# Performance work log

Hardware: AMD Instinct MI355X
Metric: run time of the kernel (lower is better)

The kernel has to match this reference:

```python
import jax, jax.numpy as jnp
import numpy as np

B, N_V, N_H, K = 16384, 4096, 1024, 3
LR, MOMENTUM, WEIGHT_DECAY = 1e-3, 0.5, 1e-4


def setup_inputs() -> dict:
    key = jax.random.key(0)
    k1, k2, k3, k4 = jax.random.split(key, 4)
    inputs = jax.random.uniform(k1, (B, N_V), dtype=jnp.float32)
    weights = jax.random.normal(k2, (N_V, N_H), dtype=jnp.float32) * 0.1
    visible_bias = jnp.ones((N_V,), jnp.float32) * 0.5
    hidden_bias = jnp.zeros((N_H,), jnp.float32)
    weights_momentum = jnp.zeros((N_V, N_H), jnp.float32)
    visible_bias_momentum = jnp.zeros((N_V,), jnp.float32)
    hidden_bias_momentum = jnp.zeros((N_H,), jnp.float32)
    # one uniform vector of length n_hidden per sampling step (matches torch code)
    rand_h0 = jax.random.uniform(k3, (N_H,), dtype=jnp.float32)
    rand_hk = jax.random.uniform(k4, (K, N_H), dtype=jnp.float32)
    return {
        "inputs": inputs,
        "weights": weights,
        "visible_bias": visible_bias,
        "hidden_bias": hidden_bias,
        "weights_momentum": weights_momentum,
        "visible_bias_momentum": visible_bias_momentum,
        "hidden_bias_momentum": hidden_bias_momentum,
        "rand_h0": rand_h0,
        "rand_hk": rand_hk,
    }


def reference(inputs, weights, visible_bias, hidden_bias,
              weights_momentum, visible_bias_momentum, hidden_bias_momentum,
              rand_h0, rand_hk):
    dtype = inputs.dtype

    def sample_hidden(v):  # [B,V] -> [B,H]
        return jax.nn.sigmoid(v @ weights + hidden_bias)

    def sample_visible(h):  # [B,H] -> [B,V]
        return jax.nn.sigmoid(h @ weights.T + visible_bias)

    # positive phase
    pos_hidden_probs = sample_hidden(inputs)                      # [B,H]
    pos_hidden_acts = (pos_hidden_probs >= rand_h0).astype(dtype)  # [B,H]
    pos_associations = inputs.T @ pos_hidden_acts                 # [V,H]

    # negative phase (CD-k). NOTE: in the original torch code `hid_acts` is
    # never updated inside the k-1 loop, so every iteration recomputes the
    # identical visible_probs/hidden_probs from pos_hidden_acts; the extra
    # bernoulli draws (rand_hk) only feed hidden_acts, which is discarded.
    # The final values are therefore exactly one reconstruction step:
    neg_visible_probs = sample_visible(pos_hidden_acts)           # [B,V]
    neg_hidden_probs = sample_hidden(neg_visible_probs)           # [B,H]
    neg_associations = neg_visible_probs.T @ neg_hidden_probs     # [V,H]

    # momentum optimizer step
    batch_size = inputs.shape[0]
    w_mom = weights_momentum * MOMENTUM + (pos_associations - neg_associations)
    vb_mom = visible_bias_momentum * MOMENTUM + jnp.sum(inputs - neg_visible_probs, axis=0)
    hb_mom = hidden_bias_momentum * MOMENTUM + jnp.sum(pos_hidden_probs - neg_hidden_probs, axis=0)

    new_weights = weights + w_mom * (LR / batch_size)
    new_weights = new_weights - new_weights * WEIGHT_DECAY
    new_visible_bias = visible_bias + vb_mom * (LR / batch_size)
    new_hidden_bias = hidden_bias + hb_mom * (LR / batch_size)

    # reconstruction error (original has a bug using builtin `input`; intended `inputs`)
    error = jnp.sum((inputs - neg_visible_probs) ** 2)
    return (error, new_weights, new_visible_bias, new_hidden_bias)
```

## Files before the change

### kernel.cpp

```cpp
#include <hip/hip_runtime.h>
#include <hip/hip_bf16.h>

#define DEV __device__ __forceinline__

typedef __attribute__((ext_vector_type(8))) short bhalf8;
typedef __attribute__((ext_vector_type(4))) float floatx4;
typedef unsigned short ushort_t;

constexpr int NB = 16384;
constexpr int NV = 4096;
constexpr int NH = 1024;
constexpr float MOM = 0.5f;
constexpr float WD  = 1e-4f;
constexpr float LRB = 1e-3f / 16384.0f;

constexpr int BUF_SHORTS = 12288;
constexpr int LDS_SHORTS = 3 * BUF_SHORTS;
constexpr size_t LDS_BYTES = LDS_SHORTS * 2 + 1024 + 64;

DEV unsigned short f2bf(float f) {
  unsigned u = __builtin_bit_cast(unsigned, f);
  u += 0x7FFFu + ((u >> 16) & 1u);
  return (unsigned short)(u >> 16);
}
DEV float bf2f(unsigned short u) {
  unsigned x = ((unsigned)u) << 16;
  return __builtin_bit_cast(float, x);
}
DEV float sigm(float x) { return 1.0f / (1.0f + __expf(-x)); }

DEV void gl16(const ushort_t* g, ushort_t* l) {
  __builtin_amdgcn_global_load_lds(
      (const __attribute__((address_space(1))) void*)g,
      (__attribute__((address_space(3))) void*)l,
      16, 0, 0);
}

struct TransLds { unsigned U[64 * 33]; };

DEV void trans_store(TransLds& T, const bhalf8& ra, const bhalf8& rb, int a, int e) {
  const unsigned* ua = (const unsigned*)&ra;
  const unsigned* ub = (const unsigned*)&rb;
#pragma unroll
  for (int c2 = 0; c2 < 4; ++c2) {
    unsigned lo = __builtin_amdgcn_perm(ub[c2], ua[c2], 0x05040100u);
    unsigned hi = __builtin_amdgcn_perm(ub[c2], ua[c2], 0x07060302u);
    T.U[(e * 8 + 2 * c2) * 33 + a] = lo;
    T.U[(e * 8 + 2 * c2 + 1) * 33 + a] = hi;
  }
}

DEV void trans_flush(const TransLds& T, ushort_t* __restrict__ oT,
                     int c0, int r0, int R, int tid) {
  const int g = tid >> 2, f = tid & 3;
  unsigned w[8];
#pragma unroll
  for (int i = 0; i < 8; ++i) w[i] = T.U[g * 33 + f * 8 + i];
  ushort_t* dst = oT + (size_t)(c0 + g) * R + r0 + f * 16;
  *(bhalf8*)dst = *(const bhalf8*)&w[0];
  *(bhalf8*)(dst + 8) = *(const bhalf8*)&w[4];
}

__global__ void prep_cvt_t(const float* __restrict__ in,
                           ushort_t* __restrict__ obf,
                           ushort_t* __restrict__ oT, int R, int C,
                           float* __restrict__ pin) {
  __shared__ TransLds T;
  __shared__ float wp[4][64];
  const int c0 = blockIdx.x * 64, r0 = blockIdx.y * 64;
  const int tid = threadIdx.x;
  const int a = tid >> 3, e = tid & 7;
  const int rA = r0 + 2 * a, cB = c0 + e * 8;

  const float* pA = in + (size_t)rA * C + cB;
  const float* pB = pA + C;
  floatx4 a0 = *(const floatx4*)pA, a1 = *(const floatx4*)(pA + 4);
  floatx4 b0 = *(const floatx4*)pB, b1 = *(const floatx4*)(pB + 4);

  bhalf8 ra, rb;
#pragma unroll
  for (int j = 0; j < 4; ++j) {
    ra[j] = (short)f2bf(a0[j]); ra[4 + j] = (short)f2bf(a1[j]);
    rb[j] = (short)f2bf(b0[j]); rb[4 + j] = (short)f2bf(b1[j]);
  }
  *(bhalf8*)(obf + (size_t)rA * C + cB) = ra;
  *(bhalf8*)(obf + (size_t)(rA + 1) * C + cB) = rb;

  if (pin) {
    float ps[8];
#pragma unroll
    for (int j = 0; j < 4; ++j) { ps[j] = a0[j] + b0[j]; ps[4 + j] = a1[j] + b1[j]; }
#pragma unroll
    for (int j = 0; j < 8; ++j) {
      ps[j] += __shfl_xor(ps[j], 8);
      ps[j] += __shfl_xor(ps[j], 16);
      ps[j] += __shfl_xor(ps[j], 32);
    }
    const int wid = tid >> 6, lane = tid & 63;
    if (lane < 8) {
#pragma unroll
      for (int j = 0; j < 8; ++j) wp[wid][lane * 8 + j] = ps[j];
    }
  }

  trans_store(T, ra, rb, a, e);
  __syncthreads();
  trans_flush(T, oT, c0, r0, R, tid);
  if (pin && tid < 64) {
    pin[(size_t)blockIdx.y * C + c0 + tid] =
        wp[0][tid] + wp[1][tid] + wp[2][tid] + wp[3][tid];
  }
}

__global__ void transb(const ushort_t* __restrict__ in,
                       ushort_t* __restrict__ out, int R, int C) {
  __shared__ TransLds T;
  const int c0 = blockIdx.x * 64, r0 = blockIdx.y * 64;
  const int tid = threadIdx.x;
  const int a = tid >> 3, e = tid & 7;
  const int rA = r0 + 2 * a, cB = c0 + e * 8;
  bhalf8 ra = *(const bhalf8*)(in + (size_t)rA * C + cB);
  bhalf8 rb = *(const bhalf8*)(in + (size_t)(rA + 1) * C + cB);
  trans_store(T, ra, rb, a, e);
  __syncthreads();
  trans_flush(T, out, c0, r0, R, tid);
}

DEV void core(const ushort_t* __restrict__ Ap,
              const ushort_t* __restrict__ Bp,
              size_t ldA, size_t ldB, int nt,
              ushort_t* Lp, int wid, int lane, int wm, int wn,
              floatx4 (&acc)[8][4]) {
  const int lr = lane & 15, kg = lane >> 4;
  const int sslot = ((lane & 3) ^ (((lane & 32) ? 2 : 0) | ((lane & 8) ? 1 : 0))) * 8;
  const ushort_t* gA = Ap + (size_t)(wid * 16 + (lane >> 2)) * ldA + sslot;
  const ushort_t* gB = Bp + (size_t)(wid * 16 + (lane >> 2)) * ldB + sslot;
  const int rslot = ((kg ^ (((lr & 8) ? 2 : 0) | ((lr & 2) ? 1 : 0))) * 8);
  const int aoff = (wm * 128 + lr) * 32 + rslot;
  const int boff = 8192 + (wn * 64 + lr) * 32 + rslot;

  auto stage = [&](int buf, int t) {
    const ushort_t* a = gA + (size_t)t * 32;
    const ushort_t* b = gB + (size_t)t * 32;
    ushort_t* LA = Lp + buf * BUF_SHORTS + wid * 512;
    ushort_t* LB = LA + 8192;
#pragma unroll
    for (int i = 0; i < 4; ++i) gl16(a + (size_t)(i * 64) * ldA, LA + i * 2048);
#pragma unroll
    for (int i = 0; i < 2; ++i) gl16(b + (size_t)(i * 64) * ldB, LB + i * 2048);
  };

  stage(0, 0);
  stage(1, 1);
  int cur = 0, pre = 2;
  for (int t = 0; t < nt; ++t) {
    if (t + 1 < nt) asm volatile("s_waitcnt vmcnt(6)" ::: "memory");
    else            asm volatile("s_waitcnt vmcnt(0)" ::: "memory");
    asm volatile("s_barrier" ::: "memory");
    if (t + 2 < nt) stage(pre, t + 2);
    const ushort_t* aB = Lp + cur * BUF_SHORTS + aoff;
    const ushort_t* bB = Lp + cur * BUF_SHORTS + boff;
    bhalf8 fa[8], fb[4];
#pragma unroll
    for (int m = 0; m < 8; ++m) fa[m] = *(const bhalf8*)(aB + m * 512);
#pragma unroll
    for (int n = 0; n < 4; ++n) fb[n] = *(const bhalf8*)(bB + n * 512);
    asm volatile("s_waitcnt lgkmcnt(0)" ::: "memory");
    __builtin_amdgcn_sched_barrier(0);
    __builtin_amdgcn_s_setprio(1);
#pragma unroll
    for (int m = 0; m < 8; ++m)
#pragma unroll
      for (int n = 0; n < 4; ++n)
        acc[m][n] = __builtin_amdgcn_mfma_f32_16x16x32_bf16(fa[m], fb[n], acc[m][n], 0, 0, 0);
    __builtin_amdgcn_s_setprio(0);
    if (++cur == 3) cur = 0;
    if (++pre == 3) pre = 0;
  }
}

template <int MODE>
__global__ __launch_bounds__(256, 2)
void gemm_fused256(const ushort_t* __restrict__ Ab,
                   const ushort_t* __restrict__ Bb,
                   int N, int K,
                   const float* __restrict__ bias,
                   const float* __restrict__ rand_h0,
                   ushort_t* __restrict__ Pout,
                   float* __restrict__ colpart,
                   const ushort_t* __restrict__ inbf,
                   float* __restrict__ err_accum) {
  extern __shared__ ushort_t Lsh[];
  const int tid = threadIdx.x;
  const int wid = tid >> 6, lane = tid & 63;
  const int wm = wid >> 1, wn = wid & 1;
  const int lr = lane & 15, kg = lane >> 4;

  const int nwg = gridDim.x * gridDim.y;
  const int id = blockIdx.y * gridDim.x + blockIdx.x;
  const int sid = (id & 7) * (nwg >> 3) + (id >> 3);
  const int n0 = (sid % gridDim.x) * 128;
  const int my = sid / gridDim.x;
  const int m0 = my * 256;

  floatx4 acc[8][4] = {};
  core(Ab + (size_t)m0 * K, Bb + (size_t)n0 * K, K, K, K / 32,
       Lsh, wid, lane, wm, wn, acc);

  __syncthreads();
  ushort_t* Rt = Lsh;
  float* colp = (float*)(Lsh + LDS_SHORTS);
  float* ered = colp + 256;
#pragma unroll
  for (int ni = 0; ni < 4; ++ni) {
    const int lcol = wn * 64 + ni * 16 + lr;
    const int col = n0 + lcol;
    const float b = bias[col];
    const float r0 = (MODE == 0) ? rand_h0[col] : 0.0f;
    float cs = 0.0f;
#pragma unroll
    for (int mi = 0; mi < 8; ++mi) {
      const int lrow = wm * 128 + mi * 16 + kg * 4;
#pragma unroll
      for (int r = 0; r < 4; ++r) {
        const float p = sigm(acc[mi][ni][r] + b);
        cs += p;
        ushort_t ov;
        if (MODE == 0) ov = (p >= r0) ? (ushort_t)0x3F80u : (ushort_t)0u;
        else           ov = f2bf(p);
        Rt[(lrow + r) * 132 + lcol] = ov;
      }
    }
    cs += __shfl_xor(cs, 16);
    cs += __shfl_xor(cs, 32);
    if (kg == 0) colp[wm * 128 + lcol] = cs;
  }
  __syncthreads();
  if (tid < 128) colpart[(size_t)my * N + n0 + tid] = colp[tid] + colp[128 + tid];
  float esum = 0.0f;
  const int c8 = (tid & 15) * 8;
  const int rb = tid >> 4;
#pragma unroll
  for (int it = 0; it < 16; ++it) {
    const int lrow = it * 16 + rb;
    bhalf8 v = *(const bhalf8*)&Rt[lrow * 132 + c8];
    const size_t g = (size_t)(m0 + lrow) * N + n0 + c8;
    *(bhalf8*)&Pout[g] = v;
    if (MODE == 1) {
      bhalf8 iv = *(const bhalf8*)&inbf[g];
#pragma unroll
      for (int j = 0; j < 8; ++j) {
        const float d = bf2f((ushort_t)iv[j]) - bf2f((ushort_t)v[j]);
        esum += d * d;
      }
    }
  }
  if (MODE == 1) {
    esum += __shfl_xor(esum, 1);
    esum += __shfl_xor(esum, 2);
    esum += __shfl_xor(esum, 4);
    esum += __shfl_xor(esum, 8);
    esum += __shfl_xor(esum, 16);
    esum += __shfl_xor(esum, 32);
    if (lane == 0) ered[wid] = esum;
    __syncthreads();
    if (tid == 0) atomicAdd(err_accum, ered[0] + ered[1] + ered[2] + ered[3]);
  }
}

__global__ __launch_bounds__(256, 2)
void gemm_nt_dual(const ushort_t* __restrict__ A1, const ushort_t* __restrict__ B1,
                  const ushort_t* __restrict__ A2, const ushort_t* __restrict__ B2,
                  float* __restrict__ outd) {
  extern __shared__ ushort_t Lsh[];
  const int tid = threadIdx.x;
  const int wid = tid >> 6, lane = tid & 63;
  const int wm = wid >> 1, wn = wid & 1;
  const int lr = lane & 15, kg = lane >> 4;

  const int bid = blockIdx.x;
  const int r = bid & 127;
  const int m0 = (r & 15) * 256;
  const int n0 = (r >> 4) * 128;
  const int z  = bid >> 7;
  const size_t kb0 = (size_t)z * (NB / 4);
  constexpr int NT = (NB / 4) / 32;

  floatx4 acc[8][4] = {};
  core(A1 + (size_t)m0 * NB + kb0, B1 + (size_t)n0 * NB + kb0, NB, NB, NT,
       Lsh, wid, lane, wm, wn, acc);
  __syncthreads();
#pragma unroll
  for (int m = 0; m < 8; ++m)
#pragma unroll
    for (int n = 0; n < 4; ++n)
#pragma unroll
      for (int j = 0; j < 4; ++j) acc[m][n][j] = -acc[m][n][j];
  core(A2 + (size_t)m0 * NB + kb0, B2 + (size_t)n0 * NB + kb0, NB, NB, NT,
       Lsh, wid, lane, wm, wn, acc);
  float* od = outd + (size_t)z * NV * NH;
#pragma unroll
  for (int mi = 0; mi < 8; ++mi) {
    const int rowb = m0 + wm * 128 + mi * 16 + kg * 4;
#pragma unroll
    for (int ni = 0; ni < 4; ++ni) {
      const int col = n0 + wn * 64 + ni * 16 + lr;
#pragma unroll
      for (int r2 = 0; r2 < 4; ++r2)
        od[(size_t)(rowb + r2) * NH + col] = -acc[mi][ni][r2];
    }
  }
}

__global__ void wupdate_kernel(const float* __restrict__ W, const float* __restrict__ wm,
                               const float* __restrict__ diff, float* __restrict__ outW) {
  const int i = blockIdx.x * blockDim.x + threadIdx.x;
  constexpr size_t SL = (size_t)NV * NH / 4;
  const floatx4 w = ((const floatx4*)W)[i];
  const floatx4 m = ((const floatx4*)wm)[i];
  const floatx4 a = ((const floatx4*)diff)[i];
  const floatx4 b = ((const floatx4*)diff)[i + SL];
  const floatx4 c = ((const floatx4*)diff)[i + 2 * SL];
  const floatx4 d = ((const floatx4*)diff)[i + 3 * SL];
  floatx4 o;
#pragma unroll
  for (int j = 0; j < 4; ++j)
    o[j] = (w[j] + (m[j] * MOM + (a[j] + b[j]) + (c[j] + d[j])) * LRB) * (1.0f - WD);
  ((floatx4*)outW)[i] = o;
}

__global__ void biaserr_kernel(const float* __restrict__ vb, const float* __restrict__ vbm,
                               const float* __restrict__ pin, const float* __restrict__ pnvp,
                               const float* __restrict__ hb, const float* __restrict__ hbm,
                               const float* __restrict__ pphp, const float* __restrict__ pnhp,
                               const float* __restrict__ err, float* __restrict__ out) {
  const int i = blockIdx.x * blockDim.x + threadIdx.x;
  if (i < NV) {
    float s_in = 0.0f, s_nvp = 0.0f;
    for (int r = 0; r < NB / 64; ++r) s_in += pin[(size_t)r * NV + i];
    for (int r = 0; r < NB / 256; ++r) s_nvp += pnvp[(size_t)r * NV + i];
    out[1 + (size_t)NV * NH + i] = vb[i] + (vbm[i] * MOM + (s_in - s_nvp)) * LRB;
  }
  if (i < NH) {
    float s_php = 0.0f, s_nhp = 0.0f;
    for (int r = 0; r < NB / 256; ++r) {
      s_php += pphp[(size_t)r * NH + i];
      s_nhp += pnhp[(size_t)r * NH + i];
    }
    out[1 + (size_t)NV * NH + NV + i] = hb[i] + (hbm[i] * MOM + (s_php - s_nhp)) * LRB;
  }
  if (i == 0) out[0] = err[0];
}

extern "C" void kernel_launch(void* const* d_in, const int* in_sizes, int n_in,
                              void* d_out, int out_size, void* d_ws, size_t ws_size,
                              hipStream_t stream) {
  const float* inputs  = (const float*)d_in[0];
  const float* W       = (const float*)d_in[1];
  const float* vb      = (const float*)d_in[2];
  const float* hb      = (const float*)d_in[3];
  const float* wmom    = (const float*)d_in[4];
  const float* vbmom   = (const float*)d_in[5];
  const float* hbmom   = (const float*)d_in[6];
  const float* rand_h0 = (const float*)d_in[7];

  hipFuncSetAttribute((const void*)gemm_fused256<0>, hipFuncAttributeMaxDynamicSharedMemorySize, (int)LDS_BYTES);
  hipFuncSetAttribute((const void*)gemm_fused256<1>, hipFuncAttributeMaxDynamicSharedMemorySize, (int)LDS_BYTES);
  hipFuncSetAttribute((const void*)gemm_fused256<2>, hipFuncAttributeMaxDynamicSharedMemorySize, (int)LDS_BYTES);
  hipFuncSetAttribute((const void*)gemm_nt_dual, hipFuncAttributeMaxDynamicSharedMemorySize, (int)LDS_BYTES);

  char* ws = (char*)d_ws;
  size_t off = 0;
  auto take = [&](size_t b) { size_t r = off; off = (off + b + 1023) & ~(size_t)1023; return r; };
  ushort_t* Wbf   = (ushort_t*)(ws + take((size_t)NV * NH * 2));
  ushort_t* WT    = (ushort_t*)(ws + take((size_t)NV * NH * 2));
  ushort_t* inbf  = (ushort_t*)(ws + take((size_t)NB * NV * 2));
  ushort_t* inT   = (ushort_t*)(ws + take((size_t)NB * NV * 2));
  ushort_t* nvp   = (ushort_t*)(ws + take((size_t)NB * NV * 2));
  ushort_t* nvpT  = (ushort_t*)(ws + take((size_t)NB * NV * 2));
  ushort_t* acts  = (ushort_t*)(ws + take((size_t)NB * NH * 2));
  ushort_t* actsT = (ushort_t*)(ws + take((size_t)NB * NH * 2));
  ushort_t* nhpT  = (ushort_t*)(ws + take((size_t)NB * NH * 2));
  float* pin  = (float*)(ws + take((size_t)(NB / 64) * NV * 4));
  float* pnvp = (float*)(ws + take((size_t)(NB / 256) * NV * 4));
  float* pphp = (float*)(ws + take((size_t)(NB / 256) * NH * 4));
  float* pnhp = (float*)(ws + take((size_t)(NB / 256) * NH * 4));
  float* errp = (float*)(ws + take(64));

  ushort_t* nhp = acts;
  float* diff   = (float*)inbf;

  hipMemsetAsync(errp, 0, 64, stream);

  prep_cvt_t<<<dim3(NV / 64, NB / 64), 256, 0, stream>>>(inputs, inbf, inT, NB, NV, pin);
  prep_cvt_t<<<dim3(NH / 64, NV / 64), 256, 0, stream>>>(W, Wbf, WT, NV, NH, nullptr);

  gemm_fused256<0><<<dim3(NH / 128, NB / 256), 256, LDS_BYTES, stream>>>(
      inbf, WT, NH, NV, hb, rand_h0, acts, pphp, nullptr, nullptr);
  transb<<<dim3(NH / 64, NB / 64), 256, 0, stream>>>(acts, actsT, NB, NH);

  gemm_fused256<1><<<dim3(NV / 128, NB / 256), 256, LDS_BYTES, stream>>>(
      acts, Wbf, NV, NH, vb, nullptr, nvp, pnvp, inbf, errp);
  transb<<<dim3(NV / 64, NB / 64), 256, 0, stream>>>(nvp, nvpT, NB, NV);

  gemm_fused256<2><<<dim3(NH / 128, NB / 256), 256, LDS_BYTES, stream>>>(
      nvp, WT, NH, NV, hb, nullptr, nhp, pnhp, nullptr, nullptr);
  transb<<<dim3(NH / 64, NB / 64), 256, 0, stream>>>(nhp, nhpT, NB, NH);

  gemm_nt_dual<<<dim3(512), 256, LDS_BYTES, stream>>>(inT, actsT, nvpT, nhpT, diff);

  wupdate_kernel<<<dim3((NV * NH / 4) / 256), 256, 0, stream>>>(W, wmom, diff, (float*)d_out + 1);
  biaserr_kernel<<<dim3(16), 256, 0, stream>>>(vb, vbmom, pin, pnvp, hb, hbmom,
                                               pphp, pnhp, errp, (float*)d_out);
}
```

Baseline: 981.3 us.

## Fuse transposed output writes into GEMM epilogues and drop transpose kernels

Each fused GEMM epilogue now also writes the transposed bf16 activations/probabilities directly through an LDS staging tile. This removes the three separate transpose kernels and their extra global read/write passes. Mode 2 also skips writing the untransposed hidden-prob output, which is only needed in transposed form. The trade-offs are recomputing the sigmoid a second time in the epilogue, extra barriers, and strided column-major global stores with 256-element runs.

```diff
diff --git a/kernel.cpp b/kernel.cpp
--- a/kernel.cpp
+++ b/kernel.cpp
@@ -110,20 +110,6 @@
     pin[(size_t)blockIdx.y * C + c0 + tid] =
         wp[0][tid] + wp[1][tid] + wp[2][tid] + wp[3][tid];
   }
-}
-
-__global__ void transb(const ushort_t* __restrict__ in,
-                       ushort_t* __restrict__ out, int R, int C) {
-  __shared__ TransLds T;
-  const int c0 = blockIdx.x * 64, r0 = blockIdx.y * 64;
-  const int tid = threadIdx.x;
-  const int a = tid >> 3, e = tid & 7;
-  const int rA = r0 + 2 * a, cB = c0 + e * 8;
-  bhalf8 ra = *(const bhalf8*)(in + (size_t)rA * C + cB);
-  bhalf8 rb = *(const bhalf8*)(in + (size_t)(rA + 1) * C + cB);
-  trans_store(T, ra, rb, a, e);
-  __syncthreads();
-  trans_flush(T, out, c0, r0, R, tid);
 }
 
 DEV void core(const ushort_t* __restrict__ Ap,
@@ -187,6 +173,7 @@
                    const float* __restrict__ bias,
                    const float* __restrict__ rand_h0,
                    ushort_t* __restrict__ Pout,
+                   ushort_t* __restrict__ PoutT,
                    float* __restrict__ colpart,
                    const ushort_t* __restrict__ inbf,
                    float* __restrict__ err_accum) {
@@ -225,10 +212,12 @@
       for (int r = 0; r < 4; ++r) {
         const float p = sigm(acc[mi][ni][r] + b);
         cs += p;
-        ushort_t ov;
-        if (MODE == 0) ov = (p >= r0) ? (ushort_t)0x3F80u : (ushort_t)0u;
-        else           ov = f2bf(p);
-        Rt[(lrow + r) * 132 + lcol] = ov;
+        if (MODE != 2) {
+          ushort_t ov;
+          if (MODE == 0) ov = (p >= r0) ? (ushort_t)0x3F80u : (ushort_t)0u;
+          else           ov = f2bf(p);
+          Rt[(lrow + r) * 132 + lcol] = ov;
+        }
       }
     }
     cs += __shfl_xor(cs, 16);
@@ -237,34 +226,69 @@
   }
   __syncthreads();
   if (tid < 128) colpart[(size_t)my * N + n0 + tid] = colp[tid] + colp[128 + tid];
-  float esum = 0.0f;
-  const int c8 = (tid & 15) * 8;
-  const int rb = tid >> 4;
-#pragma unroll
-  for (int it = 0; it < 16; ++it) {
-    const int lrow = it * 16 + rb;
-    bhalf8 v = *(const bhalf8*)&Rt[lrow * 132 + c8];
-    const size_t g = (size_t)(m0 + lrow) * N + n0 + c8;
-    *(bhalf8*)&Pout[g] = v;
+  if (MODE != 2) {
+    float esum = 0.0f;
+    const int c8 = (tid & 15) * 8;
+    const int rb = tid >> 4;
+#pragma unroll
+    for (int it = 0; it < 16; ++it) {
+      const int lrow = it * 16 + rb;
+      bhalf8 v = *(const bhalf8*)&Rt[lrow * 132 + c8];
+      const size_t g = (size_t)(m0 + lrow) * N + n0 + c8;
+      *(bhalf8*)&Pout[g] = v;
+      if (MODE == 1) {
+        bhalf8 iv = *(const bhalf8*)&inbf[g];
+#pragma unroll
+        for (int j = 0; j < 8; ++j) {
+          const float d = bf2f((ushort_t)iv[j]) - bf2f((ushort_t)v[j]);
+          esum += d * d;
+        }
+      }
+    }
     if (MODE == 1) {
-      bhalf8 iv = *(const bhalf8*)&inbf[g];
-#pragma unroll
-      for (int j = 0; j < 8; ++j) {
-        const float d = bf2f((ushort_t)iv[j]) - bf2f((ushort_t)v[j]);
-        esum += d * d;
+      esum += __shfl_xor(esum, 1);
+      esum += __shfl_xor(esum, 2);
+      esum += __shfl_xor(esum, 4);
+      esum += __shfl_xor(esum, 8);
+      esum += __shfl_xor(esum, 16);
+      esum += __shfl_xor(esum, 32);
+      if (lane == 0) ered[wid] = esum;
+      __syncthreads();
+      if (tid == 0) atomicAdd(err_accum, ered[0] + ered[1] + ered[2] + ered[3]);
+    }
+  }
+  __syncthreads();
+  unsigned* CTu = (unsigned*)Lsh;
+#pragma unroll
+  for (int ni = 0; ni < 4; ++ni) {
+    const int lcol = wn * 64 + ni * 16 + lr;
+    const int col = n0 + lcol;
+    const float b = bias[col];
+    const float r0 = (MODE == 0) ? rand_h0[col] : 0.0f;
+#pragma unroll
+    for (int mi = 0; mi < 8; ++mi) {
+      const int lrow = wm * 128 + mi * 16 + kg * 4;
+      ushort_t ov[4];
+#pragma unroll
+      for (int r = 0; r < 4; ++r) {
+        const float p = sigm(acc[mi][ni][r] + b);
+        if (MODE == 0) ov[r] = (p >= r0) ? (ushort_t)0x3F80u : (ushort_t)0u;
+        else           ov[r] = f2bf(p);
       }
-    }
-  }
-  if (MODE == 1) {
-    esum += __shfl_xor(esum, 1);
-    esum += __shfl_xor(esum, 2);
-    esum += __shfl_xor(esum, 4);
-    esum += __shfl_xor(esum, 8);
-    esum += __shfl_xor(esum, 16);
-    esum += __shfl_xor(esum, 32);
-    if (lane == 0) ered[wid] = esum;
-    __syncthreads();
-    if (tid == 0) atomicAdd(err_accum, ered[0] + ered[1] + ered[2] + ered[3]);
+      CTu[lcol * 130 + (lrow >> 1)]     = (unsigned)ov[0] | ((unsigned)ov[1] << 16);
+      CTu[lcol * 130 + (lrow >> 1) + 1] = (unsigned)ov[2] | ((unsigned)ov[3] << 16);
+    }
+  }
+  __syncthreads();
+  {
+    const int c = tid >> 1, h = tid & 1;
+    const unsigned* src = CTu + c * 130 + h * 64;
+    ushort_t* dst = PoutT + (size_t)(n0 + c) * NB + m0 + h * 128;
+#pragma unroll
+    for (int i = 0; i < 16; ++i) {
+      unsigned w4[4] = {src[i * 4], src[i * 4 + 1], src[i * 4 + 2], src[i * 4 + 3]};
+      *(bhalf8*)(dst + i * 8) = *(const bhalf8*)w4;
+    }
   }
 }
 
@@ -387,8 +411,7 @@
   float* pnhp = (float*)(ws + take((size_t)(NB / 256) * NH * 4));
   float* errp = (float*)(ws + take(64));
 
-  ushort_t* nhp = acts;
-  float* diff   = (float*)inbf;
+  float* diff = (float*)inbf;
 
   hipMemsetAsync(errp, 0, 64, stream);
 
@@ -396,16 +419,13 @@
   prep_cvt_t<<<dim3(NH / 64, NV / 64), 256, 0, stream>>>(W, Wbf, WT, NV, NH, nullptr);
 
   gemm_fused256<0><<<dim3(NH / 128, NB / 256), 256, LDS_BYTES, stream>>>(
-      inbf, WT, NH, NV, hb, rand_h0, acts, pphp, nullptr, nullptr);
-  transb<<<dim3(NH / 64, NB / 64), 256, 0, stream>>>(acts, actsT, NB, NH);
+      inbf, WT, NH, NV, hb, rand_h0, acts, actsT, pphp, nullptr, nullptr);
 
   gemm_fused256<1><<<dim3(NV / 128, NB / 256), 256, LDS_BYTES, stream>>>(
-      acts, Wbf, NV, NH, vb, nullptr, nvp, pnvp, inbf, errp);
-  transb<<<dim3(NV / 64, NB / 64), 256, 0, stream>>>(nvp, nvpT, NB, NV);
+      acts, Wbf, NV, NH, vb, nullptr, nvp, nvpT, pnvp, inbf, errp);
 
   gemm_fused256<2><<<dim3(NH / 128, NB / 256), 256, LDS_BYTES, stream>>>(
-      nvp, WT, NH, NV, hb, nullptr, nhp, pnhp, nullptr, nullptr);
-  transb<<<dim3(NH / 64, NB / 64), 256, 0, stream>>>(nhp, nhpT, NB, NH);
+      nvp, WT, NH, NV, hb, nullptr, nullptr, nhpT, pnhp, nullptr, nullptr);
 
   gemm_nt_dual<<<dim3(512), 256, LDS_BYTES, stream>>>(inT, actsT, nvpT, nhpT, diff);
 
```

New measurement: 1.060 ms. 1.08x slower.
